# Kernel optimization log

Measured on AMD Instinct MI355X. Metric: run time of the kernel, lower is better.

The kernel has to match this reference:

```python
import jax, jax.numpy as jnp
import numpy as np

B, S, D = 4, 2048, 1024
N, K = 65536, 16

def setup_inputs() -> dict:
    key = jax.random.key(0)
    k1, k2, k3, k4, k5 = jax.random.split(key, 5)
    x = jax.random.normal(k1, (B, S, D), dtype=jnp.float32)
    emb = jax.random.normal(k2, (N, D), dtype=jnp.float32)
    w = jax.random.normal(k3, (N, D), dtype=jnp.float32)
    gate = jax.random.uniform(k4, (B, S, K), dtype=jnp.float32)
    top_k_idx = jax.random.randint(k5, (B, S, K), 0, N, dtype=jnp.int32)
    return {"x": x, "emb": emb, "w": w, "gate": gate, "top_k_idx": top_k_idx}

def reference(x, emb, w, gate, top_k_idx):
    # Gather only the k active neuron rows per token from each shared pool.
    sel_emb = emb[top_k_idx]                                   # [B,S,k,D]
    sel_w = w[top_k_idx]                                       # [B,S,k,D]
    # 'sense': per-token dot with each selected emb row.
    activations = jnp.einsum('bsd,bskd->bsk', x, sel_emb)      # [B,S,k]
    gated = activations * gate                                 # [B,S,k]
    # 'emit': gated weighted combine of selected w rows.
    return jnp.einsum('bsk,bskd->bsd', gated, sel_w)           # [B,S,D]
```

## Files before the change

kernel.cpp:

```cpp
#include <hip/hip_runtime.h>

#define TOKENS 8192
#define DIM    1024
#define TOPK   16
#define NTHREADS 256

__global__ __launch_bounds__(NTHREADS) void sense_kernel(
    const float* __restrict__ x,
    const float* __restrict__ emb,
    const float* __restrict__ gate,
    const int*   __restrict__ idx,
    float*       __restrict__ gated)
{
    const int t   = blockIdx.x;
    const int tid = threadIdx.x;

    __shared__ float4 sx[DIM / 4];
    __shared__ int    sidx[TOPK];

    if (tid < TOPK) sidx[tid] = idx[(size_t)t * TOPK + tid];
    sx[tid] = reinterpret_cast<const float4*>(x + (size_t)t * DIM)[tid];
    __syncthreads();

    const int k = tid >> 4;
    const int j = tid & 15;
    const float4* row = reinterpret_cast<const float4*>(
        emb + (size_t)sidx[k] * DIM);

    float acc = 0.f;
    #pragma unroll
    for (int i = 0; i < 16; ++i) {
        const float4 e  = row[j + 16 * i];
        const float4 xv = sx[j + 16 * i];
        acc += e.x * xv.x + e.y * xv.y + e.z * xv.z + e.w * xv.w;
    }

    acc += __shfl_xor(acc, 1, 64);
    acc += __shfl_xor(acc, 2, 64);
    acc += __shfl_xor(acc, 4, 64);
    acc += __shfl_xor(acc, 8, 64);

    if (j == 0)
        gated[(size_t)t * TOPK + k] = acc * gate[(size_t)t * TOPK + k];
}

__global__ __launch_bounds__(NTHREADS) void emit_kernel(
    const float* __restrict__ w,
    const float* __restrict__ gated,
    const int*   __restrict__ idx,
    float*       __restrict__ out)
{
    const int t   = blockIdx.x;
    const int tid = threadIdx.x;

    __shared__ int   sidx[TOPK];
    __shared__ float sg[TOPK];

    if (tid < TOPK) {
        sidx[tid] = idx[(size_t)t * TOPK + tid];
        sg[tid]   = gated[(size_t)t * TOPK + tid];
    }
    __syncthreads();

    float ax = 0.f, ay = 0.f, az = 0.f, aw = 0.f;
    #pragma unroll
    for (int k = 0; k < TOPK; ++k) {
        const float g = sg[k];
        const float4 wv = reinterpret_cast<const float4*>(
            w + (size_t)sidx[k] * DIM)[tid];
        ax += g * wv.x; ay += g * wv.y; az += g * wv.z; aw += g * wv.w;
    }
    reinterpret_cast<float4*>(out + (size_t)t * DIM)[tid] =
        make_float4(ax, ay, az, aw);
}

extern "C" void kernel_launch(void* const* d_in, const int* in_sizes, int n_in,
                              void* d_out, int out_size, void* d_ws, size_t ws_size,
                              hipStream_t stream) {
    const float* x    = (const float*)d_in[0];
    const float* emb  = (const float*)d_in[1];
    const float* w    = (const float*)d_in[2];
    const float* gate = (const float*)d_in[3];
    const int*   idx  = (const int*)d_in[4];
    float*       out  = (float*)d_out;
    float*       gated = (float*)d_ws;

    sense_kernel<<<TOKENS, NTHREADS, 0, stream>>>(x, emb, gate, idx, gated);
    emit_kernel <<<TOKENS, NTHREADS, 0, stream>>>(w, gated, idx, out);
}
```

Measured before the change: 169.6 us.

## Fuse sense and emit kernels into one per-token kernel

Merges the two kernels into one block per token: the gated activations stay in shared memory and are never written to or read back from a workspace, which also drops a launch. The x row is read straight from global memory (16 threads per row share it through cache) instead of being staged in LDS. The emit loop is hand-unrolled into two batches of eight row loads, with indices read as int4, so more gathers are in flight at once. The cost is higher register pressure, and the emit gathers can no longer overlap with other blocks' sense phase across kernels.

```diff
diff --git a/kernel.cpp b/kernel.cpp
--- a/kernel.cpp
+++ b/kernel.cpp
@@ -3,36 +3,34 @@
 #define TOKENS 8192
 #define DIM    1024
 #define TOPK   16
-#define NTHREADS 256
+#define NT     256
 
-__global__ __launch_bounds__(NTHREADS) void sense_kernel(
+__global__ __launch_bounds__(NT) void kc_fused_kernel(
     const float* __restrict__ x,
     const float* __restrict__ emb,
+    const float* __restrict__ w,
     const float* __restrict__ gate,
     const int*   __restrict__ idx,
-    float*       __restrict__ gated)
+    float*       __restrict__ out)
 {
     const int t   = blockIdx.x;
     const int tid = threadIdx.x;
+    const int k   = tid >> 4;
+    const int j   = tid & 15;
 
-    __shared__ float4 sx[DIM / 4];
-    __shared__ int    sidx[TOPK];
+    __shared__ float sg[TOPK];
 
-    if (tid < TOPK) sidx[tid] = idx[(size_t)t * TOPK + tid];
-    sx[tid] = reinterpret_cast<const float4*>(x + (size_t)t * DIM)[tid];
-    __syncthreads();
+    const int row = idx[t * TOPK + k];
 
-    const int k = tid >> 4;
-    const int j = tid & 15;
-    const float4* row = reinterpret_cast<const float4*>(
-        emb + (size_t)sidx[k] * DIM);
+    const float4* e  = reinterpret_cast<const float4*>(emb) + (size_t)row * (DIM / 4) + j;
+    const float4* xv = reinterpret_cast<const float4*>(x)   + (size_t)t   * (DIM / 4) + j;
 
     float acc = 0.f;
     #pragma unroll
     for (int i = 0; i < 16; ++i) {
-        const float4 e  = row[j + 16 * i];
-        const float4 xv = sx[j + 16 * i];
-        acc += e.x * xv.x + e.y * xv.y + e.z * xv.z + e.w * xv.w;
+        const float4 ev = e[16 * i];
+        const float4 xw = xv[16 * i];
+        acc += ev.x * xw.x + ev.y * xw.y + ev.z * xw.z + ev.w * xw.w;
     }
 
     acc += __shfl_xor(acc, 1, 64);
@@ -41,35 +39,52 @@
     acc += __shfl_xor(acc, 8, 64);
 
     if (j == 0)
-        gated[(size_t)t * TOPK + k] = acc * gate[(size_t)t * TOPK + k];
-}
-
-__global__ __launch_bounds__(NTHREADS) void emit_kernel(
-    const float* __restrict__ w,
-    const float* __restrict__ gated,
-    const int*   __restrict__ idx,
-    float*       __restrict__ out)
-{
-    const int t   = blockIdx.x;
-    const int tid = threadIdx.x;
-
-    __shared__ int   sidx[TOPK];
-    __shared__ float sg[TOPK];
-
-    if (tid < TOPK) {
-        sidx[tid] = idx[(size_t)t * TOPK + tid];
-        sg[tid]   = gated[(size_t)t * TOPK + tid];
-    }
+        sg[k] = acc * gate[t * TOPK + k];
     __syncthreads();
 
+    const int4* iv = reinterpret_cast<const int4*>(idx + t * TOPK);
+    const int4 i0 = iv[0], i1 = iv[1], i2 = iv[2], i3 = iv[3];
+
+    const float4* wb = reinterpret_cast<const float4*>(w);
+
     float ax = 0.f, ay = 0.f, az = 0.f, aw = 0.f;
-    #pragma unroll
-    for (int k = 0; k < TOPK; ++k) {
-        const float g = sg[k];
-        const float4 wv = reinterpret_cast<const float4*>(
-            w + (size_t)sidx[k] * DIM)[tid];
-        ax += g * wv.x; ay += g * wv.y; az += g * wv.z; aw += g * wv.w;
+    {
+        const float4 r0 = wb[(size_t)i0.x * (DIM/4) + tid];
+        const float4 r1 = wb[(size_t)i0.y * (DIM/4) + tid];
+        const float4 r2 = wb[(size_t)i0.z * (DIM/4) + tid];
+        const float4 r3 = wb[(size_t)i0.w * (DIM/4) + tid];
+        const float4 r4 = wb[(size_t)i1.x * (DIM/4) + tid];
+        const float4 r5 = wb[(size_t)i1.y * (DIM/4) + tid];
+        const float4 r6 = wb[(size_t)i1.z * (DIM/4) + tid];
+        const float4 r7 = wb[(size_t)i1.w * (DIM/4) + tid];
+        ax += sg[0]*r0.x; ay += sg[0]*r0.y; az += sg[0]*r0.z; aw += sg[0]*r0.w;
+        ax += sg[1]*r1.x; ay += sg[1]*r1.y; az += sg[1]*r1.z; aw += sg[1]*r1.w;
+        ax += sg[2]*r2.x; ay += sg[2]*r2.y; az += sg[2]*r2.z; aw += sg[2]*r2.w;
+        ax += sg[3]*r3.x; ay += sg[3]*r3.y; az += sg[3]*r3.z; aw += sg[3]*r3.w;
+        ax += sg[4]*r4.x; ay += sg[4]*r4.y; az += sg[4]*r4.z; aw += sg[4]*r4.w;
+        ax += sg[5]*r5.x; ay += sg[5]*r5.y; az += sg[5]*r5.z; aw += sg[5]*r5.w;
+        ax += sg[6]*r6.x; ay += sg[6]*r6.y; az += sg[6]*r6.z; aw += sg[6]*r6.w;
+        ax += sg[7]*r7.x; ay += sg[7]*r7.y; az += sg[7]*r7.z; aw += sg[7]*r7.w;
     }
+    {
+        const float4 r0 = wb[(size_t)i2.x * (DIM/4) + tid];
+        const float4 r1 = wb[(size_t)i2.y * (DIM/4) + tid];
+        const float4 r2 = wb[(size_t)i2.z * (DIM/4) + tid];
+        const float4 r3 = wb[(size_t)i2.w * (DIM/4) + tid];
+        const float4 r4 = wb[(size_t)i3.x * (DIM/4) + tid];
+        const float4 r5 = wb[(size_t)i3.y * (DIM/4) + tid];
+        const float4 r6 = wb[(size_t)i3.z * (DIM/4) + tid];
+        const float4 r7 = wb[(size_t)i3.w * (DIM/4) + tid];
+        ax += sg[8] *r0.x; ay += sg[8] *r0.y; az += sg[8] *r0.z; aw += sg[8] *r0.w;
+        ax += sg[9] *r1.x; ay += sg[9] *r1.y; az += sg[9] *r1.z; aw += sg[9] *r1.w;
+        ax += sg[10]*r2.x; ay += sg[10]*r2.y; az += sg[10]*r2.z; aw += sg[10]*r2.w;
+        ax += sg[11]*r3.x; ay += sg[11]*r3.y; az += sg[11]*r3.z; aw += sg[11]*r3.w;
+        ax += sg[12]*r4.x; ay += sg[12]*r4.y; az += sg[12]*r4.z; aw += sg[12]*r4.w;
+        ax += sg[13]*r5.x; ay += sg[13]*r5.y; az += sg[13]*r5.z; aw += sg[13]*r5.w;
+        ax += sg[14]*r6.x; ay += sg[14]*r6.y; az += sg[14]*r6.z; aw += sg[14]*r6.w;
+        ax += sg[15]*r7.x; ay += sg[15]*r7.y; az += sg[15]*r7.z; aw += sg[15]*r7.w;
+    }
+
     reinterpret_cast<float4*>(out + (size_t)t * DIM)[tid] =
         make_float4(ax, ay, az, aw);
 }
@@ -83,8 +98,6 @@
     const float* gate = (const float*)d_in[3];
     const int*   idx  = (const int*)d_in[4];
     float*       out  = (float*)d_out;
-    float*       gated = (float*)d_ws;
 
-    sense_kernel<<<TOKENS, NTHREADS, 0, stream>>>(x, emb, gate, idx, gated);
-    emit_kernel <<<TOKENS, NTHREADS, 0, stream>>>(w, gated, idx, out);
+    kc_fused_kernel<<<TOKENS, NT, 0, stream>>>(x, emb, w, gate, idx, out);
 }
```

Result: faster. 163.0 us (-3.9%).
